# Kernel optimization log

Measured on AMD Instinct MI355X. Metric: run time of the kernel, lower is better.

Reference implementation:

```python
import jax, jax.numpy as jnp
import numpy as np

N_NODES = 100000


def gcn_conv(x, edge_index, W, b):
    # PyG GCNConv: add self-loops, symmetric normalization D^-1/2 (A+I) D^-1/2, transform, aggregate, bias.
    src, dst = edge_index[0], edge_index[1]
    n = x.shape[0]
    xw = x @ W  # [N, out] transform before propagate (PyG order)
    # degree with self-loops (count edges by target + 1)
    deg = jax.ops.segment_sum(jnp.ones_like(dst, dtype=xw.dtype), dst, num_segments=n) + 1.0
    dinv = jax.lax.rsqrt(deg)  # deg >= 1, safe
    norm = dinv[src] * dinv[dst]  # [E]
    msgs = xw[src] * norm[:, None]  # [E, out] gathered, normalized messages
    agg = jax.ops.segment_sum(msgs, dst, num_segments=n)
    # self-loop contribution: norm_ii = dinv_i^2 = 1/deg_i
    agg = agg + xw * (dinv * dinv)[:, None]
    return agg + b


def setup_inputs() -> dict:
    key = jax.random.key(0)
    ks = jax.random.split(key, 8)
    in_c, h1, h2, out_c = 128, 71, 82, 1
    x = jax.random.normal(ks[0], (N_NODES, in_c), dtype=jnp.float32)
    edge_index = jax.random.randint(ks[1], (2, 1600000), 0, N_NODES, dtype=jnp.int64)
    def glorot(k, fan_in, fan_out):
        s = jnp.sqrt(6.0 / (fan_in + fan_out))
        return jax.random.uniform(k, (fan_in, fan_out), jnp.float32, -s, s)
    return {
        "x": x,
        "edge_index": edge_index,
        "W1": glorot(ks[2], in_c, h1), "b1": jnp.zeros((h1,), jnp.float32),
        "W2": glorot(ks[3], h1, h2), "b2": jnp.zeros((h2,), jnp.float32),
        "W3": glorot(ks[4], h2, out_c), "b3": jnp.zeros((out_c,), jnp.float32),
    }


def reference(x, edge_index, W1, b1, W2, b2, W3, b3):
    h = jax.nn.relu(gcn_conv(x, edge_index, W1, b1))
    h = gcn_conv(h, edge_index, W2, b2)  # note: no relu after conv2 in source
    return gcn_conv(h, edge_index, W3, b3)
```

## Files before the change

### kernel.cpp

```cpp
#include <hip/hip_runtime.h>
#include <hip/hip_fp16.h>

#define NNODES 100000
#define NB 391
#define BSHIFT 8
#define BMASK 255
#define BCAP 4864
#define WT_LD 136

typedef _Float16 half8 __attribute__((ext_vector_type(8)));
typedef float floatx4 __attribute__((ext_vector_type(4)));

__global__ __launch_bounds__(1024) void binAP_kernel(
        const int* __restrict__ src, const int* __restrict__ dst,
        int* __restrict__ bcnt, unsigned* __restrict__ bdata, int E,
        const float* __restrict__ W1, const float* __restrict__ W2,
        const float* __restrict__ b2, const float* __restrict__ W3,
        float* __restrict__ w23, __half* __restrict__ Wt) {
    if (blockIdx.x == NB) {
        int k = threadIdx.x;
        if (k < 71) {
            float a = 0.f;
            for (int j = 0; j < 82; ++j) a += W2[k * 82 + j] * W3[j];
            w23[k] = a;
        } else if (k == 71) {
            float a = 0.f;
            for (int j = 0; j < 82; ++j) a += b2[j] * W3[j];
            w23[71] = a;
        }
        for (int i = threadIdx.x; i < 80 * WT_LD; i += 1024) {
            int nn = i / WT_LD, kk = i - nn * WT_LD;
            float v = (nn < 71 && kk < 128) ? W1[kk * 71 + nn] : 0.f;
            Wt[i] = __float2half(v);
        }
        return;
    }
    __shared__ unsigned sorted[4096];
    __shared__ unsigned short bkt[4096];
    __shared__ int hist[NB];
    __shared__ int sbase[NB];
    __shared__ int gb[NB];
    __shared__ int wsum[8];
    int tid = threadIdx.x;
    const int BATCH = 4096;
    for (int base = blockIdx.x * BATCH; base < E; base += NB * BATCH) {
        int bE = min(BATCH, E - base);
        for (int i = tid; i < NB; i += 1024) hist[i] = 0;
        __syncthreads();
        int s[4], d[4], rk[4], bb[4];
        int cnt = 0;
        if (bE == BATCH) {
            int4 sv = ((const int4*)(src + base))[tid];
            int4 dv = ((const int4*)(dst + base))[tid];
            s[0] = sv.x; d[0] = dv.x; s[1] = sv.y; d[1] = dv.y;
            s[2] = sv.z; d[2] = dv.z; s[3] = sv.w; d[3] = dv.w;
            cnt = 4;
#pragma unroll
            for (int k = 0; k < 4; ++k) {
                bb[k] = d[k] >> BSHIFT;
                rk[k] = atomicAdd(&hist[bb[k]], 1);
            }
        } else {
#pragma unroll
            for (int k = 0; k < 4; ++k) {
                int idx = base + k * 1024 + tid;
                if (idx < E) {
                    s[cnt] = src[idx];
                    d[cnt] = dst[idx];
                    bb[cnt] = d[cnt] >> BSHIFT;
                    rk[cnt] = atomicAdd(&hist[bb[cnt]], 1);
                    ++cnt;
                }
            }
        }
        __syncthreads();
        if (tid < 448) {
            int v = (tid < NB) ? hist[tid] : 0;
            int lane = tid & 63;
            int incl = v;
#pragma unroll
            for (int off = 1; off < 64; off <<= 1) {
                int t = __shfl_up(incl, off);
                if (lane >= off) incl += t;
            }
            if (tid < NB) sbase[tid] = incl - v;
            if (lane == 63) wsum[tid >> 6] = incl;
        }
        __syncthreads();
        if (tid == 0) {
            int acc = 0;
#pragma unroll
            for (int w = 0; w < 7; ++w) { int t = wsum[w]; wsum[w] = acc; acc += t; }
        }
        __syncthreads();
        if (tid < NB) {
            sbase[tid] += wsum[tid >> 6];
            int c = hist[tid];
            gb[tid] = (c > 0) ? atomicAdd(&bcnt[tid], c) : 0;
        }
        __syncthreads();
        for (int k = 0; k < cnt; ++k) {
            int pos = sbase[bb[k]] + rk[k];
            sorted[pos] = ((unsigned)s[k] << BSHIFT) | ((unsigned)d[k] & BMASK);
            bkt[pos] = (unsigned short)bb[k];
        }
        __syncthreads();
        for (int i = tid; i < bE; i += 1024) {
            int bb2 = bkt[i];
            int lo = gb[bb2] + (i - sbase[bb2]);
            if (lo < BCAP)
                bdata[(size_t)bb2 * BCAP + lo] = sorted[i];
        }
        __syncthreads();
    }
}

__global__ __launch_bounds__(1024) void binB2_kernel(
        const int* __restrict__ bcnt, const unsigned* __restrict__ bdata,
        int* __restrict__ deg, int* __restrict__ end_off, float* __restrict__ dinv,
        int* __restrict__ csr, int n) {
    __shared__ unsigned sorted[BCAP];
    __shared__ int hist[256];
    __shared__ int nstart[256];
    __shared__ int wsum[4];
    __shared__ int scal[2];
    int b = blockIdx.x;
    int tid = threadIdx.x;
    if (tid < 64) {
        int s = 0;
        int lo = tid * 7, hi = min(tid * 7 + 7, b);
        for (int i = lo; i < hi; ++i) s += min(bcnt[i], BCAP);
#pragma unroll
        for (int off = 32; off; off >>= 1) s += __shfl_down(s, off);
        if (tid == 0) { scal[0] = s; scal[1] = min(bcnt[b], BCAP); }
    }
    if (tid < 256) hist[tid] = 0;
    __syncthreads();
    int cnt = scal[1];
    int base = scal[0];
    const unsigned* p = bdata + (size_t)b * BCAP;
    unsigned ev[5]; int rv[5];
    int ec = 0;
    for (int i = tid; i < cnt; i += 1024) {
        unsigned e = p[i];
        ev[ec] = e;
        rv[ec] = atomicAdd(&hist[e & BMASK], 1);
        ++ec;
    }
    __syncthreads();
    if (tid < 256) {
        int v = hist[tid];
        int lane = tid & 63;
        int incl = v;
#pragma unroll
        for (int off = 1; off < 64; off <<= 1) {
            int t = __shfl_up(incl, off);
            if (lane >= off) incl += t;
        }
        nstart[tid] = incl - v;
        if (lane == 63) wsum[tid >> 6] = incl;
    }
    __syncthreads();
    if (tid == 0) {
        int acc = 0;
#pragma unroll
        for (int w = 0; w < 4; ++w) { int t = wsum[w]; wsum[w] = acc; acc += t; }
    }
    __syncthreads();
    if (tid < 256) {
        int excl = nstart[tid] + wsum[tid >> 6];
        nstart[tid] = excl;
        int v = hist[tid];
        int node = (b << BSHIFT) + tid;
        if (node < n) {
            deg[node] = v;
            end_off[node] = base + excl + v;
            dinv[node] = rsqrtf((float)v + 1.0f);
        }
    }
    __syncthreads();
    for (int k = 0; k < ec; ++k) {
        unsigned e = ev[k];
        sorted[nstart[e & BMASK] + rv[k]] = e >> BSHIFT;
    }
    __syncthreads();
    for (int i = tid; i < cnt; i += 1024) csr[base + i] = (int)sorted[i];
}

__global__ __launch_bounds__(256) void xform_mfma(
        const float* __restrict__ x, const __half* __restrict__ Wt,
        const float* __restrict__ scale, __half* __restrict__ msgA,
        __half* __restrict__ msgB, int n) {
    __shared__ __half Wsh[80 * WT_LD];
    {
        const uint4* sp = (const uint4*)Wt;
        uint4* dp = (uint4*)Wsh;
        for (int i = threadIdx.x; i < (80 * WT_LD * 2) / 16; i += blockDim.x) dp[i] = sp[i];
    }
    __syncthreads();
    int lane = threadIdx.x & 63;
    int m = lane & 15, q = lane >> 4;
    int gw = (blockIdx.x * blockDim.x + threadIdx.x) >> 6;
    int nw = (gridDim.x * blockDim.x) >> 6;
    int nrt = n >> 4;
    for (int rt = gw; rt < nrt; rt += nw) {
        int rb = rt << 4;
        const float* xr = x + (size_t)(rb + m) * 128 + q * 8;
        floatx4 acc[5];
#pragma unroll
        for (int t = 0; t < 5; ++t) acc[t] = (floatx4){0.f, 0.f, 0.f, 0.f};
#pragma unroll
        for (int ks = 0; ks < 4; ++ks) {
            float4 f0 = *(const float4*)(xr + ks * 32);
            float4 f1 = *(const float4*)(xr + ks * 32 + 4);
            half8 a;
            a[0] = (_Float16)f0.x; a[1] = (_Float16)f0.y;
            a[2] = (_Float16)f0.z; a[3] = (_Float16)f0.w;
            a[4] = (_Float16)f1.x; a[5] = (_Float16)f1.y;
            a[6] = (_Float16)f1.z; a[7] = (_Float16)f1.w;
#pragma unroll
            for (int t = 0; t < 5; ++t) {
                half8 b = *(const half8*)&Wsh[(t * 16 + m) * WT_LD + ks * 32 + q * 8];
                acc[t] = __builtin_amdgcn_mfma_f32_16x16x32_f16(a, b, acc[t], 0, 0, 0);
            }
        }
        float sc[4];
#pragma unroll
        for (int r = 0; r < 4; ++r) sc[r] = scale[rb + q * 4 + r];
#pragma unroll
        for (int t = 0; t < 5; ++t) {
            int col = t * 16 + m;
#pragma unroll
            for (int r = 0; r < 4; ++r) {
                __half hv = __float2half(acc[t][r] * sc[r]);
                int row = rb + q * 4 + r;
                if (t < 4) {
                    msgA[(size_t)row * 64 + col] = hv;
                } else if (m < 8) {
                    msgB[(size_t)row * 8 + m] = hv;
                }
            }
        }
    }
}

__global__ __launch_bounds__(256) void gather_fused(
        const __half* __restrict__ msgA, const __half* __restrict__ msgB,
        const int* __restrict__ csr, const int* __restrict__ end_off,
        const int* __restrict__ deg, const float* __restrict__ dinv,
        const float* __restrict__ b, const float* __restrict__ w23,
        float* __restrict__ g2, int n) {
    int lane = threadIdx.x & 63;
    int li = lane & 7;
    int wid = (blockIdx.x * blockDim.x + threadIdx.x) >> 6;
    int nwaves = (gridDim.x * blockDim.x) >> 6;
    float bA[8], wA[8];
#pragma unroll
    for (int j = 0; j < 8; ++j) { bA[j] = b[8 * li + j]; wA[j] = w23[8 * li + j]; }
    float bB = (li < 7) ? b[64 + li] : 0.f;
    float wB = (li < 7) ? w23[64 + li] : 0.f;
    const char* mA = (const char*)msgA;
    const char* mB = (const char*)msgB;
    unsigned laneA   = (unsigned)(li << 4);
    unsigned laneBof = (unsigned)((li >> 1) << 2);
    unsigned laneBsh = (unsigned)((li & 1) << 4);
    int ntiles = n >> 3;
    for (int tile = wid; tile < ntiles; tile += nwaves) {
        int node = (tile << 3) + (lane >> 3);
        int ee = end_off[node];
        int d = deg[node];
        int st = ee - d;
        float dv = dinv[node];
        int tmax = d;
        tmax = max(tmax, __shfl_xor(tmax, 8));
        tmax = max(tmax, __shfl_xor(tmax, 16));
        tmax = max(tmax, __shfl_xor(tmax, 32));
        tmax = __builtin_amdgcn_readfirstlane(tmax);
        float acc[8];
#pragma unroll
        for (int j = 0; j < 8; ++j) acc[j] = 0.f;
        float bsum = 0.f;
        int c0 = csr[(0 < d) ? st + 0 : 0];
        int c1 = csr[(1 < d) ? st + 1 : 0];
        int c2 = csr[(2 < d) ? st + 2 : 0];
        int c3 = csr[(3 < d) ? st + 3 : 0];
        int c4 = csr[(4 < d) ? st + 4 : 0];
        int c5 = csr[(5 < d) ? st + 5 : 0];
        int c6 = csr[(6 < d) ? st + 6 : 0];
        int c7 = csr[(7 < d) ? st + 7 : 0];
        unsigned i0 = (unsigned)((0 < d) ? c0 : node);
        unsigned i1 = (unsigned)((1 < d) ? c1 : node);
        unsigned i2 = (unsigned)((2 < d) ? c2 : node);
        unsigned i3 = (unsigned)((3 < d) ? c3 : node);
        half8 r0 = *(const half8*)(mA + ((i0 << 7) | laneA));
        half8 r1 = *(const half8*)(mA + ((i1 << 7) | laneA));
        half8 r2 = *(const half8*)(mA + ((i2 << 7) | laneA));
        half8 r3 = *(const half8*)(mA + ((i3 << 7) | laneA));
        unsigned w0 = *(const unsigned*)(mB + ((i0 << 4) | laneBof));
        unsigned w1 = *(const unsigned*)(mB + ((i1 << 4) | laneBof));
        unsigned w2 = *(const unsigned*)(mB + ((i2 << 4) | laneBof));
        unsigned w3 = *(const unsigned*)(mB + ((i3 << 4) | laneBof));
        for (int i = 0; i <= tmax; i += 4) {
            int n0 = csr[(i + 8  < d) ? st + i + 8  : 0];
            int n1 = csr[(i + 9  < d) ? st + i + 9  : 0];
            int n2 = csr[(i + 10 < d) ? st + i + 10 : 0];
            int n3 = csr[(i + 11 < d) ? st + i + 11 : 0];
            unsigned j0 = (unsigned)((i + 4 < d) ? c4 : node);
            unsigned j1 = (unsigned)((i + 5 < d) ? c5 : node);
            unsigned j2 = (unsigned)((i + 6 < d) ? c6 : node);
            unsigned j3 = (unsigned)((i + 7 < d) ? c7 : node);
            half8 s0 = *(const half8*)(mA + ((j0 << 7) | laneA));
            half8 s1 = *(const half8*)(mA + ((j1 << 7) | laneA));
            half8 s2 = *(const half8*)(mA + ((j2 << 7) | laneA));
            half8 s3 = *(const half8*)(mA + ((j3 << 7) | laneA));
            unsigned u0 = *(const unsigned*)(mB + ((j0 << 4) | laneBof));
            unsigned u1 = *(const unsigned*)(mB + ((j1 << 4) | laneBof));
            unsigned u2 = *(const unsigned*)(mB + ((j2 << 4) | laneBof));
            unsigned u3 = *(const unsigned*)(mB + ((j3 << 4) | laneBof));
            if (i <= d) {
#pragma unroll
                for (int j = 0; j < 8; ++j) acc[j] += (float)r0[j];
                unsigned short us = (unsigned short)(w0 >> laneBsh);
                _Float16 hf; __builtin_memcpy(&hf, &us, 2);
                bsum += (float)hf;
            }
            if (i + 1 <= d) {
#pragma unroll
                for (int j = 0; j < 8; ++j) acc[j] += (float)r1[j];
                unsigned short us = (unsigned short)(w1 >> laneBsh);
                _Float16 hf; __builtin_memcpy(&hf, &us, 2);
                bsum += (float)hf;
            }
            if (i + 2 <= d) {
#pragma unroll
                for (int j = 0; j < 8; ++j) acc[j] += (float)r2[j];
                unsigned short us = (unsigned short)(w2 >> laneBsh);
                _Float16 hf; __builtin_memcpy(&hf, &us, 2);
                bsum += (float)hf;
            }
            if (i + 3 <= d) {
#pragma unroll
                for (int j = 0; j < 8; ++j) acc[j] += (float)r3[j];
                unsigned short us = (unsigned short)(w3 >> laneBsh);
                _Float16 hf; __builtin_memcpy(&hf, &us, 2);
                bsum += (float)hf;
            }
            c4 = n0; c5 = n1; c6 = n2; c7 = n3;
            r0 = s0; r1 = s1; r2 = s2; r3 = s3;
            w0 = u0; w1 = u1; w2 = u2; w3 = u3;
        }
        float p = 0.f;
#pragma unroll
        for (int j = 0; j < 8; ++j) p += fmaxf(dv * acc[j] + bA[j], 0.f) * wA[j];
        p += fmaxf(dv * bsum + bB, 0.f) * wB;
        p += __shfl_xor(p, 1);
        p += __shfl_xor(p, 2);
        p += __shfl_xor(p, 4);
        if (li == 0) g2[node] = dv * p;
    }
}

__global__ void sgather_q(const float* __restrict__ g2, const int* __restrict__ csr,
                          const int* __restrict__ end_off, const int* __restrict__ deg,
                          const float* __restrict__ dinv, const float* __restrict__ w23,
                          float* __restrict__ q, int n) {
    float bw = w23[71];
    int lane = threadIdx.x & 63;
    int g = lane >> 4, k = lane & 15;
    int wid = (blockIdx.x * blockDim.x + threadIdx.x) >> 6;
    int nw = (gridDim.x * blockDim.x) >> 6;
    for (int i0 = wid * 4; i0 < n; i0 += nw * 4) {
        int i = i0 + g;
        float acc = 0.f;
        float dv = 0.f;
        if (i < n) {
            int end = end_off[i];
            int cnt = deg[i];
            int start = end - cnt;
            dv = dinv[i];
            int e = k;
            for (; e + 16 < cnt; e += 32) {
                int a0 = csr[start + e];
                int a1 = csr[start + e + 16];
                acc += g2[a0] + g2[a1];
            }
            for (; e < cnt; e += 16) acc += g2[csr[start + e]];
        }
        acc += __shfl_down(acc, 8, 16);
        acc += __shfl_down(acc, 4, 16);
        acc += __shfl_down(acc, 2, 16);
        acc += __shfl_down(acc, 1, 16);
        if (i < n && k == 0) q[i] = dv * (dv * (acc + g2[i]) + bw);
    }
}

__global__ void sgather_out(const float* __restrict__ q, const int* __restrict__ csr,
                            const int* __restrict__ end_off, const int* __restrict__ deg,
                            const float* __restrict__ dinv, const float* __restrict__ b3,
                            float* __restrict__ out, int n) {
    float bv = b3[0];
    int lane = threadIdx.x & 63;
    int g = lane >> 4, k = lane & 15;
    int wid = (blockIdx.x * blockDim.x + threadIdx.x) >> 6;
    int nw = (gridDim.x * blockDim.x) >> 6;
    for (int i0 = wid * 4; i0 < n; i0 += nw * 4) {
        int i = i0 + g;
        float acc = 0.f;
        float dv = 0.f;
        if (i < n) {
            int end = end_off[i];
            int cnt = deg[i];
            int start = end - cnt;
            dv = dinv[i];
            int e = k;
            for (; e + 16 < cnt; e += 32) {
                int a0 = csr[start + e];
                int a1 = csr[start + e + 16];
                acc += q[a0] + q[a1];
            }
            for (; e < cnt; e += 16) acc += q[csr[start + e]];
        }
        acc += __shfl_down(acc, 8, 16);
        acc += __shfl_down(acc, 4, 16);
        acc += __shfl_down(acc, 2, 16);
        acc += __shfl_down(acc, 1, 16);
        if (i < n && k == 0) out[i] = dv * (acc + q[i]) + bv;
    }
}

extern "C" void kernel_launch(void* const* d_in, const int* in_sizes, int n_in,
                              void* d_out, int out_size, void* d_ws, size_t ws_size,
                              hipStream_t stream) {
    const float* x  = (const float*)d_in[0];
    const int*   ei = (const int*)d_in[1];
    const float* W1 = (const float*)d_in[2];
    const float* b1 = (const float*)d_in[3];
    const float* W2 = (const float*)d_in[4];
    const float* b2 = (const float*)d_in[5];
    const float* W3 = (const float*)d_in[6];
    const float* b3 = (const float*)d_in[7];
    float* out = (float*)d_out;

    const int n = NNODES;
    const int E = in_sizes[1] / 2;
    const int* src = ei;
    const int* dst = ei + E;

    float* ws     = (float*)d_ws;
    float* dinv   = ws;
    int*   deg_i  = (int*)(ws + n);
    int*   offs   = deg_i + n;
    int*   bcnt   = offs + n;
    float* w23    = (float*)(bcnt + 512);
    __half* Wt    = (__half*)(w23 + 80);
    float* g2     = (float*)(Wt + 11008);
    float* q      = g2 + n;
    int*   csr    = (int*)(q + n);
    __half* msgA  = (__half*)(csr + E + 16);
    __half* msgB  = msgA + (size_t)n * 64;
    unsigned* bdata = (unsigned*)(msgB + (size_t)n * 8);

    hipMemsetAsync(bcnt, 0, 512 * sizeof(int), stream);
    binAP_kernel<<<NB + 1, 1024, 0, stream>>>(src, dst, bcnt, bdata, E,
                                              W1, W2, b2, W3, w23, Wt);
    binB2_kernel<<<NB, 1024, 0, stream>>>(bcnt, bdata, deg_i, offs, dinv, csr, n);
    xform_mfma<<<1563, 256, 0, stream>>>(x, Wt, dinv, msgA, msgB, n);
    gather_fused<<<3125, 256, 0, stream>>>(msgA, msgB, csr, offs, deg_i, dinv, b1, w23, g2, n);
    sgather_q<<<2048, 256, 0, stream>>>(g2, csr, offs, deg_i, dinv, w23, q, n);
    sgather_out<<<2048, 256, 0, stream>>>(q, csr, offs, deg_i, dinv, b3, out, n);
}
```

Baseline: 200.5 us.

## Group nodes by degree within each bucket to balance gather wave work

binB2 now builds a per-256-node-bucket permutation that sorts nodes by in-degree (capped at 63) using a shared histogram and scan. The three gather kernels walk nodes through this permutation, so the 8 or 16 nodes sharing a wave have similar degrees and the per-wave maximum-degree loop wastes fewer lanes. The cost is an extra indirection load per node, node accesses to end_off/deg/dinv/msg that are less contiguous, and scattered output writes.

```diff
diff --git a/kernel.cpp b/kernel.cpp
--- a/kernel.cpp
+++ b/kernel.cpp
@@ -118,12 +118,14 @@
 __global__ __launch_bounds__(1024) void binB2_kernel(
         const int* __restrict__ bcnt, const unsigned* __restrict__ bdata,
         int* __restrict__ deg, int* __restrict__ end_off, float* __restrict__ dinv,
-        int* __restrict__ csr, int n) {
+        int* __restrict__ csr, int* __restrict__ perm, int n) {
     __shared__ unsigned sorted[BCAP];
     __shared__ int hist[256];
     __shared__ int nstart[256];
     __shared__ int wsum[4];
     __shared__ int scal[2];
+    __shared__ int dh[64];
+    __shared__ int dbs[64];
     int b = blockIdx.x;
     int tid = threadIdx.x;
     if (tid < 64) {
@@ -133,6 +135,7 @@
 #pragma unroll
         for (int off = 32; off; off >>= 1) s += __shfl_down(s, off);
         if (tid == 0) { scal[0] = s; scal[1] = min(bcnt[b], BCAP); }
+        dh[tid] = 0;
     }
     if (tid < 256) hist[tid] = 0;
     __syncthreads();
@@ -167,6 +170,7 @@
         for (int w = 0; w < 4; ++w) { int t = wsum[w]; wsum[w] = acc; acc += t; }
     }
     __syncthreads();
+    int dr = 0;
     if (tid < 256) {
         int excl = nstart[tid] + wsum[tid >> 6];
         nstart[tid] = excl;
@@ -176,14 +180,30 @@
             deg[node] = v;
             end_off[node] = base + excl + v;
             dinv[node] = rsqrtf((float)v + 1.0f);
-        }
-    }
-    __syncthreads();
+            dr = atomicAdd(&dh[min(v, 63)], 1);
+        }
+    }
+    __syncthreads();
+    if (tid < 64) {
+        int vv = dh[tid];
+        int incl = vv;
+#pragma unroll
+        for (int off = 1; off < 64; off <<= 1) {
+            int t = __shfl_up(incl, off);
+            if (tid >= off) incl += t;
+        }
+        dbs[tid] = incl - vv;
+    }
     for (int k = 0; k < ec; ++k) {
         unsigned e = ev[k];
         sorted[nstart[e & BMASK] + rv[k]] = e >> BSHIFT;
     }
     __syncthreads();
+    if (tid < 256) {
+        int node = (b << BSHIFT) + tid;
+        if (node < n)
+            perm[(b << BSHIFT) + dbs[min(hist[tid], 63)] + dr] = node;
+    }
     for (int i = tid; i < cnt; i += 1024) csr[base + i] = (int)sorted[i];
 }
 
@@ -248,6 +268,7 @@
         const __half* __restrict__ msgA, const __half* __restrict__ msgB,
         const int* __restrict__ csr, const int* __restrict__ end_off,
         const int* __restrict__ deg, const float* __restrict__ dinv,
+        const int* __restrict__ perm,
         const float* __restrict__ b, const float* __restrict__ w23,
         float* __restrict__ g2, int n) {
     int lane = threadIdx.x & 63;
@@ -266,7 +287,7 @@
     unsigned laneBsh = (unsigned)((li & 1) << 4);
     int ntiles = n >> 3;
     for (int tile = wid; tile < ntiles; tile += nwaves) {
-        int node = (tile << 3) + (lane >> 3);
+        int node = perm[(tile << 3) + (lane >> 3)];
         int ee = end_off[node];
         int d = deg[node];
         int st = ee - d;
@@ -362,7 +383,8 @@
 
 __global__ void sgather_q(const float* __restrict__ g2, const int* __restrict__ csr,
                           const int* __restrict__ end_off, const int* __restrict__ deg,
-                          const float* __restrict__ dinv, const float* __restrict__ w23,
+                          const float* __restrict__ dinv, const int* __restrict__ perm,
+                          const float* __restrict__ w23,
                           float* __restrict__ q, int n) {
     float bw = w23[71];
     int lane = threadIdx.x & 63;
@@ -370,10 +392,13 @@
     int wid = (blockIdx.x * blockDim.x + threadIdx.x) >> 6;
     int nw = (gridDim.x * blockDim.x) >> 6;
     for (int i0 = wid * 4; i0 < n; i0 += nw * 4) {
-        int i = i0 + g;
+        int ii = i0 + g;
         float acc = 0.f;
         float dv = 0.f;
-        if (i < n) {
+        int i = 0;
+        bool ok = ii < n;
+        if (ok) {
+            i = perm[ii];
             int end = end_off[i];
             int cnt = deg[i];
             int start = end - cnt;
@@ -390,13 +415,14 @@
         acc += __shfl_down(acc, 4, 16);
         acc += __shfl_down(acc, 2, 16);
         acc += __shfl_down(acc, 1, 16);
-        if (i < n && k == 0) q[i] = dv * (dv * (acc + g2[i]) + bw);
+        if (ok && k == 0) q[i] = dv * (dv * (acc + g2[i]) + bw);
     }
 }
 
 __global__ void sgather_out(const float* __restrict__ q, const int* __restrict__ csr,
                             const int* __restrict__ end_off, const int* __restrict__ deg,
-                            const float* __restrict__ dinv, const float* __restrict__ b3,
+                            const float* __restrict__ dinv, const int* __restrict__ perm,
+                            const float* __restrict__ b3,
                             float* __restrict__ out, int n) {
     float bv = b3[0];
     int lane = threadIdx.x & 63;
@@ -404,10 +430,13 @@
     int wid = (blockIdx.x * blockDim.x + threadIdx.x) >> 6;
     int nw = (gridDim.x * blockDim.x) >> 6;
     for (int i0 = wid * 4; i0 < n; i0 += nw * 4) {
-        int i = i0 + g;
+        int ii = i0 + g;
         float acc = 0.f;
         float dv = 0.f;
-        if (i < n) {
+        int i = 0;
+        bool ok = ii < n;
+        if (ok) {
+            i = perm[ii];
             int end = end_off[i];
             int cnt = deg[i];
             int start = end - cnt;
@@ -424,7 +453,7 @@
         acc += __shfl_down(acc, 4, 16);
         acc += __shfl_down(acc, 2, 16);
         acc += __shfl_down(acc, 1, 16);
-        if (i < n && k == 0) out[i] = dv * (acc + q[i]) + bv;
+        if (ok && k == 0) out[i] = dv * (acc + q[i]) + bv;
     }
 }
 
@@ -450,7 +479,8 @@
     float* dinv   = ws;
     int*   deg_i  = (int*)(ws + n);
     int*   offs   = deg_i + n;
-    int*   bcnt   = offs + n;
+    int*   perm   = offs + n;
+    int*   bcnt   = perm + n;
     float* w23    = (float*)(bcnt + 512);
     __half* Wt    = (__half*)(w23 + 80);
     float* g2     = (float*)(Wt + 11008);
@@ -463,9 +493,10 @@
     hipMemsetAsync(bcnt, 0, 512 * sizeof(int), stream);
     binAP_kernel<<<NB + 1, 1024, 0, stream>>>(src, dst, bcnt, bdata, E,
                                               W1, W2, b2, W3, w23, Wt);
-    binB2_kernel<<<NB, 1024, 0, stream>>>(bcnt, bdata, deg_i, offs, dinv, csr, n);
+    binB2_kernel<<<NB, 1024, 0, stream>>>(bcnt, bdata, deg_i, offs, dinv, csr, perm, n);
     xform_mfma<<<1563, 256, 0, stream>>>(x, Wt, dinv, msgA, msgB, n);
-    gather_fused<<<3125, 256, 0, stream>>>(msgA, msgB, csr, offs, deg_i, dinv, b1, w23, g2, n);
-    sgather_q<<<2048, 256, 0, stream>>>(g2, csr, offs, deg_i, dinv, w23, q, n);
-    sgather_out<<<2048, 256, 0, stream>>>(q, csr, offs, deg_i, dinv, b3, out, n);
-}
+    gather_fused<<<3125, 256, 0, stream>>>(msgA, msgB, csr, offs, deg_i, dinv, perm,
+                                           b1, w23, g2, n);
+    sgather_q<<<2048, 256, 0, stream>>>(g2, csr, offs, deg_i, dinv, perm, w23, q, n);
+    sgather_out<<<2048, 256, 0, stream>>>(q, csr, offs, deg_i, dinv, perm, b3, out, n);
+}
```

Measured after the change: 219.1 us. 9.3% more time.
